# Optimization experiments

Hardware: AMD Instinct MI355X
Metric: run time of the kernel (lower is better)

## Reference

```python
import math
import jax, jax.numpy as jnp
import numpy as np

HEADS = 8
LOG_APPROX_VAR = math.log(0.01)  # self.var = 0.01, non-trainable


def clustering(x, approx_log_var, mu, log_var, log_prior):
    """Faithful port of DisentangledAttention.clustering (mi_estimation=False).
    x: [B,H,L,D]; approx_log_var: [B,H,L]; mu/log_var: [H,C,D]; log_prior: [H,C].
    Returns (cluster_probs [B,H,L,C], kl_loss [B,1,1], div_loss [B])."""
    B, H, L, D = x.shape
    xe = x[:, :, :, None, :]                      # [B,H,L,1,D]
    mue = mu[:, None, :, :]                       # [H,1,C,D]
    alv = approx_log_var[:, :, :, None, None]     # [B,H,L,1,1]
    avar = jnp.exp(alv)
    lv = log_var[:, None, :, :]                   # [H,1,C,D]
    var = jnp.exp(lv)
    logp = jax.nn.log_softmax(log_prior, axis=-1)  # [H,C]

    mse = (xe - mue) ** 2 / var                   # [B,H,L,C,D]
    log_pdf = -0.5 * mse.sum(-1) - D * math.pi - 0.5 * lv.sum(-1)  # [B,H,L,C]
    log_pdf = log_pdf + logp[:, None, :]
    log_probs = jax.nn.log_softmax(log_pdf, axis=-1)
    probs = jnp.exp(log_probs)                    # [B,H,L,C]

    logp_b = logp[None, :, None, :]               # broadcast prior log-probs
    prior = jnp.exp(logp_b)
    # F.kl_div(log_probs, prior) = prior * (log(prior) - log_probs)
    kl = (prior * (logp_b - log_probs)).sum(-1).mean(axis=(1, 2))            # [B]
    kl = kl + 0.5 * (probs * (mse + avar / var + lv).sum(-1)).sum(-1).mean(axis=(1, 2))
    kl = kl - 0.5 * jnp.mean(((1.0 + alv).sum(-1)) * D, axis=(1, 2, 3))
    kl_loss = kl.reshape(-1, 1, 1)

    eyeL = jnp.eye(L, dtype=x.dtype)
    div = jnp.einsum('bhqc,bhkc->bhqk', probs, probs)   # [B,H,L,L]
    div = (div - eyeL) ** 2
    wmask = eyeL * 1.25 + (1.0 - eyeL) * 0.75
    div_loss = (div * wmask).mean(axis=(1, 2, 3))       # [B]
    return probs, kl_loss, div_loss


def setup_inputs() -> dict:
    k = jax.random.key(0)
    ks = jax.random.split(k, 10)
    B, L, D, H, C = 4, 1024, 512, HEADS, 8
    Dk = D // H
    lin_std = 1.0 / math.sqrt(2.0 * D)  # xavier_normal gain=1/sqrt(2)
    return {
        'query': jax.random.normal(ks[0], (B, L, D), jnp.float32),
        'key': jax.random.normal(ks[1], (B, L, D), jnp.float32),
        'value': jax.random.normal(ks[2], (B, L, D), jnp.float32),
        'padding_mask': jnp.zeros((B, 1, L), jnp.float32),
        'Wq': jax.random.normal(ks[3], (D, D), jnp.float32) * lin_std,
        'bq': jnp.zeros((D,), jnp.float32),
        'Wk': jax.random.normal(ks[4], (D, D), jnp.float32) * lin_std,
        'bk': jnp.zeros((D,), jnp.float32),
        'Wv': jax.random.normal(ks[5], (D, D), jnp.float32) * lin_std,
        'bv': jnp.zeros((D,), jnp.float32),
        'Wo': jax.random.normal(ks[6], (D, D), jnp.float32) * lin_std,
        'bo': jnp.zeros((D,), jnp.float32),
        'tok_mu': jax.random.normal(ks[7], (H, C, Dk), jnp.float32) * 0.1,
        'tok_log_var': jnp.zeros((H, C, Dk), jnp.float32),
        'tok_log_prior': jnp.full((H, C), math.log(1.0 / C), jnp.float32),
    }


def reference(query, key, value, padding_mask, Wq, bq, Wk, bk, Wv, bv, Wo, bo,
              tok_mu, tok_log_var, tok_log_prior):
    B, L, D = query.shape
    H = HEADS
    Dk = D // H

    # GMM clustering on raw (unprojected) per-head query/key, eval mode (no reparam noise)
    qh = query.reshape(B, L, H, Dk).transpose(0, 2, 1, 3)  # [B,H,L,Dk]
    kh = key.reshape(B, L, H, Dk).transpose(0, 2, 1, 3)
    alv = jnp.full((B, H, L), LOG_APPROX_VAR, dtype=query.dtype)
    probs_q, kl_q, div_q = clustering(qh, alv, tok_mu, tok_log_var, tok_log_prior)
    probs_k, kl_k, div_k = clustering(kh, alv, tok_mu, tok_log_var, tok_log_prior)

    # Disentangled mask: tokens sharing clusters attend (mask==1 means blocked)
    sim = jnp.einsum('bhqc,bhkc->bhqk', probs_q, probs_k)   # [B,H,L,L]
    cmask = jnp.clip(1.0 - sim + padding_mask[:, :, None, :], 0.0, 1.0)

    # Projections + scaled softmax attention (per softmax_attention/full_attention)
    q = (query @ Wq.T + bq).reshape(B, L, H, Dk).transpose(0, 2, 1, 3) / math.sqrt(Dk)
    kk = (key @ Wk.T + bk).reshape(B, L, H, Dk).transpose(0, 2, 1, 3)
    v = (value @ Wv.T + bv).reshape(B, L, H, Dk).transpose(0, 2, 1, 3)
    scores = jnp.einsum('bhqd,bhkd->bhqk', q, kk) + jax.lax.stop_gradient(cmask) * (-10000.0)
    attn = jax.nn.softmax(scores, axis=-1) * (1.0 - cmask)
    out = jnp.einsum('bhqk,bhkd->bhqd', attn, v).transpose(0, 2, 1, 3).reshape(B, L, D)
    out = out @ Wo.T + bo

    kl_loss = kl_q + kl_k                      # [B,1,1]
    div_loss = (div_q + div_k).reshape(-1, 1, 1)  # [B,1,1]
    return out, kl_loss, div_loss
```

## Files before the change

kernel.cpp:

```cpp
#include <hip/hip_runtime.h>
#include <hip/hip_bf16.h>
#include <math.h>

#define NB 4
#define NL 1024
#define ND 512
#define NH 8
#define NC 8
#define NDK 64

static constexpr float KL3_CONST = 115.36544595161891f;

typedef __bf16 bf16x8 __attribute__((ext_vector_type(8)));
typedef float  f32x4v __attribute__((ext_vector_type(4)));
typedef unsigned short u16x4 __attribute__((ext_vector_type(4)));
typedef unsigned short u16x8 __attribute__((ext_vector_type(8)));

__device__ __forceinline__ unsigned short bf16u(float f) {
    return __builtin_bit_cast(unsigned short, (__bf16)f);
}

struct GemmArgs {
    const void* A; const float* W; const float* bias; void* out;
    float scale; int abf; int obf; int brow; int ostr; int vmap;
};

#define GEMM_BUF 15360

__device__ __forceinline__ void gemm_body(const GemmArgs& g, unsigned char* smem)
{
    const int tid = threadIdx.x;
    int n0, m0;
    if (g.vmap) {
        const int linear = blockIdx.y * 4 + blockIdx.x;
        n0 = (linear & 31) * 128;
        m0 = (linear >> 5) * 64;
    } else {
        n0 = blockIdx.x * 128;
        m0 = blockIdx.y * 64;
    }

    const int w = tid >> 6, lane = tid & 63;
    const int r16 = lane & 15, quad = lane >> 4;
    const int arow = tid >> 2, akc = tid & 3;
    const int wrow = tid >> 1, wkc = tid & 1;

    f32x4v acc[8];
#pragma unroll
    for (int n = 0; n < 8; ++n) acc[n] = (f32x4v){0.f, 0.f, 0.f, 0.f};

    auto ldA = [&](int k0) -> u16x8 {
        if (g.abf) {
            return *(const u16x8*)((const unsigned short*)g.A + (size_t)(m0 + arow) * 512 + k0 + akc * 8);
        }
        const float* ap = (const float*)g.A + (size_t)(m0 + arow) * 512 + k0 + akc * 8;
        const float4 a0 = *(const float4*)ap, a1 = *(const float4*)(ap + 4);
        return (u16x8){ bf16u(a0.x), bf16u(a0.y), bf16u(a0.z), bf16u(a0.w),
                        bf16u(a1.x), bf16u(a1.y), bf16u(a1.z), bf16u(a1.w) };
    };
    auto ldW = [&](int k0, u16x8* dst) {
        const float* wp = (const float*)g.W + (size_t)(n0 + wrow) * 512 + k0 + wkc * 16;
        const float4 w0 = *(const float4*)wp,       w1 = *(const float4*)(wp + 4);
        const float4 w2 = *(const float4*)(wp + 8), w3 = *(const float4*)(wp + 12);
        dst[0] = (u16x8){ bf16u(w0.x), bf16u(w0.y), bf16u(w0.z), bf16u(w0.w),
                          bf16u(w1.x), bf16u(w1.y), bf16u(w1.z), bf16u(w1.w) };
        dst[1] = (u16x8){ bf16u(w2.x), bf16u(w2.y), bf16u(w2.z), bf16u(w2.w),
                          bf16u(w3.x), bf16u(w3.y), bf16u(w3.z), bf16u(w3.w) };
    };
    auto store_stage = [&](int buf, const u16x8& sa, const u16x8* sw) {
        unsigned short* As = (unsigned short*)(smem + buf * GEMM_BUF);
        unsigned short* Ws = (unsigned short*)(smem + buf * GEMM_BUF + 5120);
        *(u16x8*)(As + arow * 40 + akc * 8) = sa;
        *(u16x8*)(Ws + wrow * 40 + wkc * 16) = sw[0];
        *(u16x8*)(Ws + wrow * 40 + wkc * 16 + 8) = sw[1];
    };
    auto mfma_half = [&](int buf) {
        unsigned short* As = (unsigned short*)(smem + buf * GEMM_BUF);
        unsigned short* Ws = (unsigned short*)(smem + buf * GEMM_BUF + 5120);
        bf16x8 af = *(const bf16x8*)(As + (w * 16 + r16) * 40 + quad * 8);
#pragma unroll
        for (int ni = 0; ni < 8; ++ni) {
            bf16x8 bfr = *(const bf16x8*)(Ws + (ni * 16 + r16) * 40 + quad * 8);
            acc[ni] = __builtin_amdgcn_mfma_f32_16x16x32_bf16(af, bfr, acc[ni], 0, 0, 0);
        }
    };

    u16x8 sa0 = ldA(0),  sw0[2]; ldW(0, sw0);
    u16x8 sa1 = ldA(32), sw1[2]; ldW(32, sw1);
    store_stage(0, sa0, sw0);
    sa0 = ldA(64); ldW(64, sw0);

    for (int p = 0; p < 16; p += 2) {
        const int kbase = p * 32;
        __syncthreads();
        store_stage(1, sa1, sw1);
        if (kbase + 96 < 512) { sa1 = ldA(kbase + 96); ldW(kbase + 96, sw1); }
        mfma_half(0);

        __syncthreads();
        if (p + 2 < 16) store_stage(0, sa0, sw0);
        if (kbase + 128 < 512) { sa0 = ldA(kbase + 128); ldW(kbase + 128, sw0); }
        mfma_half(1);
    }

#pragma unroll
    for (int ni = 0; ni < 8; ++ni) {
        const int col = n0 + ni * 16 + r16;
        const float bcol = g.brow ? 0.f : g.bias[col];
#pragma unroll
        for (int i = 0; i < 4; ++i) {
            const int row = m0 + w * 16 + quad * 4 + i;
            const float bv = g.brow ? g.bias[row] : bcol;
            const float v = (acc[ni][i] + bv) * g.scale;
            if (g.obf) ((unsigned short*)g.out)[(size_t)row * g.ostr + col] = bf16u(v);
            else       ((float*)g.out)[(size_t)row * g.ostr + col] = v;
        }
    }
}

__device__ __forceinline__ void cluster_body(
    const float* __restrict__ query, const float* __restrict__ key,
    const float* __restrict__ tok_mu, const float* __restrict__ tok_log_var,
    const float* __restrict__ tok_log_prior,
    float* __restrict__ probs_q, float* __restrict__ probs_k,
    float* __restrict__ klp, float* __restrict__ divp, float* __restrict__ Gp,
    int linear, unsigned char* smem)
{
    float* mu_s    = (float*)smem;
    float* iv_s    = (float*)(smem + 2048);
    float* Pl      = (float*)(smem + 4096);
    float* Gpart   = (float*)(smem + 13312);
    float* red_s   = (float*)(smem + 14336);
    float* lvsum_s = (float*)(smem + 14368);
    float* alpha_s = (float*)(smem + 14400);
    float* logp_s  = (float*)(smem + 14432);
    float* prior_s = (float*)(smem + 14464);

    const int tid  = threadIdx.x;
    const int side = linear >> 7;
    const int rem  = linear & 127;
    const int bh   = rem >> 2, chunk = rem & 3;
    const int b    = bh >> 3, h = bh & 7;
    const int blocklin = side * 128 + bh * 4 + chunk;
    const float* src = side ? key : query;
    float* probs_out = side ? probs_k : probs_q;

    for (int i = tid; i < 512; i += 256) {
        mu_s[i] = tok_mu[h * 512 + i];
        float lv = tok_log_var[h * 512 + i];
        iv_s[i] = __expf(-lv);
    }
    if (tid < 8) {
        float ls = 0.f, al = 0.f;
        for (int d = 0; d < 64; ++d) {
            float lv = tok_log_var[(h * 8 + tid) * 64 + d];
            ls += lv;
            al += 0.01f * __expf(-lv) + lv;
        }
        lvsum_s[tid] = ls; alpha_s[tid] = al;
    }
    if (tid == 0) {
        float lp[8]; float mx = -1e30f;
        for (int c = 0; c < 8; ++c) { lp[c] = tok_log_prior[h * 8 + c]; mx = fmaxf(mx, lp[c]); }
        float se = 0.f;
        for (int c = 0; c < 8; ++c) se += __expf(lp[c] - mx);
        float lse = mx + __logf(se);
        for (int c = 0; c < 8; ++c) { logp_s[c] = lp[c] - lse; prior_s[c] = __expf(lp[c] - lse); }
    }
    __syncthreads();

    const int l = chunk * 256 + tid;
    const float4* xp = (const float4*)(src + ((size_t)(b * NL + l)) * ND + h * NDK);
    float4 xr[16];
#pragma unroll
    for (int i = 0; i < 16; ++i) xr[i] = xp[i];

    float ms[8];
#pragma unroll
    for (int c = 0; c < 8; ++c) {
        const float4* mc = (const float4*)(mu_s + c * 64);
        const float4* ic = (const float4*)(iv_s + c * 64);
        float s = 0.f;
#pragma unroll
        for (int i = 0; i < 16; ++i) {
            float4 m4 = mc[i], v4 = ic[i], x4 = xr[i];
            float dx = x4.x - m4.x; s = fmaf(dx * dx, v4.x, s);
            float dy = x4.y - m4.y; s = fmaf(dy * dy, v4.y, s);
            float dz = x4.z - m4.z; s = fmaf(dz * dz, v4.z, s);
            float dw = x4.w - m4.w; s = fmaf(dw * dw, v4.w, s);
        }
        ms[c] = s;
    }

    float lpdf[8]; float mx = -1e30f;
#pragma unroll
    for (int c = 0; c < 8; ++c) {
        lpdf[c] = -0.5f * (ms[c] + lvsum_s[c]) + logp_s[c];
        mx = fmaxf(mx, lpdf[c]);
    }
    float e[8]; float se = 0.f;
#pragma unroll
    for (int c = 0; c < 8; ++c) { e[c] = __expf(lpdf[c] - mx); se += e[c]; }
    float lse = __logf(se);
    float inv = 1.f / se;
    float p[8]; float kl1 = 0.f, kl2 = 0.f, sqq = 0.f;
#pragma unroll
    for (int c = 0; c < 8; ++c) {
        p[c] = e[c] * inv;
        float logprob = lpdf[c] - mx - lse;
        kl1 += prior_s[c] * (logp_s[c] - logprob);
        kl2 += p[c] * (ms[c] + alpha_s[c]);
        sqq = fmaf(p[c], p[c], sqq);
    }

    float* po = probs_out + ((size_t)((b * NH + h) * NL + l)) * NC;
    ((float4*)po)[0] = make_float4(p[0], p[1], p[2], p[3]);
    ((float4*)po)[1] = make_float4(p[4], p[5], p[6], p[7]);
#pragma unroll
    for (int c = 0; c < 8; ++c) Pl[tid * 9 + c] = p[c];

    float dterm = 1.25f * (sqq - 1.f) * (sqq - 1.f) - 0.75f * sqq * sqq;
    float klv = kl1 + 0.5f * kl2;
    __syncthreads();

    {
        int qt = tid >> 6, pos = tid & 63, c1 = pos >> 3, c2 = pos & 7;
        float g = 0.f;
        for (int i = 0; i < 64; ++i) {
            int ll = qt * 64 + i;
            g = fmaf(Pl[ll * 9 + c1], Pl[ll * 9 + c2], g);
        }
        Gpart[qt * 64 + pos] = g;
    }

#pragma unroll
    for (int o = 32; o > 0; o >>= 1) {
        klv   += __shfl_down(klv, o);
        dterm += __shfl_down(dterm, o);
    }
    if ((tid & 63) == 0) { red_s[tid >> 6] = klv; red_s[4 + (tid >> 6)] = dterm; }
    __syncthreads();
    if (tid == 0) {
        klp[blocklin]  = red_s[0] + red_s[1] + red_s[2] + red_s[3];
        divp[blocklin] = red_s[4] + red_s[5] + red_s[6] + red_s[7];
    }
    if (tid < 64)
        Gp[(size_t)blocklin * 64 + tid] =
            Gpart[tid] + Gpart[64 + tid] + Gpart[128 + tid] + Gpart[192 + tid];
}

__global__ __launch_bounds__(256) void fused_front(
    GemmArgs g0, GemmArgs g1, GemmArgs g2,
    const float* query, const float* key,
    const float* tok_mu, const float* tok_log_var, const float* tok_log_prior,
    float* probs_q, float* probs_k,
    float* klp, float* divp, float* Gp)
{
    __shared__ alignas(16) unsigned char smem[2 * GEMM_BUF];
    if (blockIdx.z == 3) {
        const int linear = blockIdx.y * 4 + blockIdx.x;
        cluster_body(query, key, tok_mu, tok_log_var, tok_log_prior,
                     probs_q, probs_k, klp, divp, Gp, linear, smem);
        return;
    }
    GemmArgs g = (blockIdx.z == 0) ? g0 : ((blockIdx.z == 1) ? g1 : g2);
    gemm_body(g, smem);
}

#define APAD 72

__global__ __launch_bounds__(256) void attn_mfma5_kernel(
    const unsigned short* __restrict__ qp16, const unsigned short* __restrict__ kp16,
    const unsigned short* __restrict__ vtp16,
    const float* __restrict__ probs_q, const float* __restrict__ probs_k,
    const float* __restrict__ padding_mask,
    float* __restrict__ pO, float* __restrict__ pML)
{
    const int tid = threadIdx.x, lane = tid & 63, w = tid >> 6;
    const int r16 = lane & 15, quad = lane >> 4;
    const int b = blockIdx.z >> 1, s = blockIdx.z & 1;
    const int h = blockIdx.y;
    const int qt = blockIdx.x;
    const int qbase = qt * 64;

    __shared__ alignas(16) unsigned short Ks[64 * APAD];
    __shared__ alignas(16) unsigned short Vt[64 * APAD];
    __shared__ alignas(16) unsigned short Ps[4][16 * APAD];
    __shared__ float pk_s[8 * 65];
    __shared__ float pm_s[64];

    const int c0row = tid >> 3,        c0c8 = tid & 7;
    const int c1row = (tid + 256) >> 3, c1c8 = tid & 7;
    const int pkey = tid >> 1, phalf = tid & 1;

    bf16x8 qa[2];
    {
        const unsigned short* qrow = qp16 + ((size_t)(b * NL + qbase + w * 16 + r16)) * ND + h * NDK;
        qa[0] = *(const bf16x8*)(qrow + quad * 8);
        qa[1] = *(const bf16x8*)(qrow + 32 + quad * 8);
    }
    float pq[4][8];
#pragma unroll
    for (int i = 0; i < 4; ++i) {
        const float* pr = probs_q + ((size_t)((b * NH + h) * NL + qbase + w * 16 + quad * 4 + i)) * NC;
        float4 a = ((const float4*)pr)[0], c = ((const float4*)pr)[1];
        pq[i][0] = a.x; pq[i][1] = a.y; pq[i][2] = a.z; pq[i][3] = a.w;
        pq[i][4] = c.x; pq[i][5] = c.y; pq[i][6] = c.z; pq[i][7] = c.w;
    }

    f32x4v oacc[4];
#pragma unroll
    for (int n = 0; n < 4; ++n) oacc[n] = (f32x4v){0.f, 0.f, 0.f, 0.f};
    float m_i[4] = {-1e30f, -1e30f, -1e30f, -1e30f};
    float l_i[4] = {0.f, 0.f, 0.f, 0.f};

    u16x8 rk0, rk1, rv0, rv1;
    float4 rpk;
    float rpm;

    auto stage_load = [&](int kt) {
        const int key0 = s * 512 + kt * 64;
        rk0 = *(const u16x8*)(kp16 + ((size_t)(b * NL + key0 + c0row)) * ND + h * NDK + c0c8 * 8);
        rk1 = *(const u16x8*)(kp16 + ((size_t)(b * NL + key0 + c1row)) * ND + h * NDK + c1c8 * 8);
        rv0 = *(const u16x8*)(vtp16 + ((size_t)(h * 64 + c0row)) * (NB * NL) + b * NL + key0 + c0c8 * 8);
        rv1 = *(const u16x8*)(vtp16 + ((size_t)(h * 64 + c1row)) * (NB * NL) + b * NL + key0 + c1c8 * 8);
        if (tid < 128)
            rpk = *(const float4*)(probs_k + ((size_t)((b * NH + h) * NL + key0 + pkey)) * NC + phalf * 4);
        if (tid < 64)
            rpm = padding_mask[b * NL + key0 + tid];
    };
    auto stage_store = [&]() {
        *(u16x8*)(Ks + c0row * APAD + c0c8 * 8) = rk0;
        *(u16x8*)(Ks + c1row * APAD + c1c8 * 8) = rk1;
        *(u16x8*)(Vt + c0row * APAD + c0c8 * 8) = rv0;
        *(u16x8*)(Vt + c1row * APAD + c1c8 * 8) = rv1;
        if (tid < 128) {
            pk_s[(phalf * 4 + 0) * 65 + pkey] = rpk.x;
            pk_s[(phalf * 4 + 1) * 65 + pkey] = rpk.y;
            pk_s[(phalf * 4 + 2) * 65 + pkey] = rpk.z;
            pk_s[(phalf * 4 + 3) * 65 + pkey] = rpk.w;
        }
        if (tid < 64) pm_s[tid] = rpm;
    };

    stage_load(0);
    stage_store();
    stage_load(1);

    for (int kt = 0; kt < 8; ++kt) {
        __syncthreads();

        f32x4v sacc[4];
#pragma unroll
        for (int t = 0; t < 4; ++t) {
            sacc[t] = (f32x4v){0.f, 0.f, 0.f, 0.f};
            bf16x8 kb0 = *(const bf16x8*)(Ks + (t * 16 + r16) * APAD + quad * 8);
            bf16x8 kb1 = *(const bf16x8*)(Ks + (t * 16 + r16) * APAD + 32 + quad * 8);
            sacc[t] = __builtin_amdgcn_mfma_f32_16x16x32_bf16(qa[0], kb0, sacc[t], 0, 0, 0);
            sacc[t] = __builtin_amdgcn_mfma_f32_16x16x32_bf16(qa[1], kb1, sacc[t], 0, 0, 0);
        }

        float sc[4][4], wgt[4][4];
#pragma unroll
        for (int t = 0; t < 4; ++t) {
            const int keyl = t * 16 + r16;
            float pkc[8];
#pragma unroll
            for (int c = 0; c < 8; ++c) pkc[c] = pk_s[c * 65 + keyl];
            const float pmv = pm_s[keyl];
#pragma unroll
            for (int i = 0; i < 4; ++i) {
                float sim = 0.f;
#pragma unroll
                for (int c = 0; c < 8; ++c) sim = fmaf(pq[i][c], pkc[c], sim);
                float cm = 1.f - sim + pmv;
                cm = fminf(fmaxf(cm, 0.f), 1.f);
                sc[t][i] = sacc[t][i] - 10000.f * cm;
                wgt[t][i] = 1.f - cm;
            }
        }

        float mx[4];
#pragma unroll
        for (int i = 0; i < 4; ++i)
            mx[i] = fmaxf(fmaxf(sc[0][i], sc[1][i]), fmaxf(sc[2][i], sc[3][i]));
#pragma unroll
        for (int o = 1; o < 16; o <<= 1) {
#pragma unroll
            for (int i = 0; i < 4; ++i) mx[i] = fmaxf(mx[i], __shfl_xor(mx[i], o));
        }
        float rr[4];
#pragma unroll
        for (int i = 0; i < 4; ++i) {
            const float mnew = fmaxf(m_i[i], mx[i]);
            rr[i] = __expf(m_i[i] - mnew);
            m_i[i] = mnew;
            l_i[i] *= rr[i];
        }
#pragma unroll
        for (int n = 0; n < 4; ++n) {
            oacc[n][0] *= rr[0]; oacc[n][1] *= rr[1];
            oacc[n][2] *= rr[2]; oacc[n][3] *= rr[3];
        }
        float lad[4] = {0.f, 0.f, 0.f, 0.f};
#pragma unroll
        for (int t = 0; t < 4; ++t) {
#pragma unroll
            for (int i = 0; i < 4; ++i) {
                const float p = __expf(sc[t][i] - m_i[i]);
                lad[i] += p;
                Ps[w][(quad * 4 + i) * APAD + t * 16 + r16] = bf16u(p * wgt[t][i]);
            }
        }
#pragma unroll
        for (int o = 1; o < 16; o <<= 1) {
#pragma unroll
            for (int i = 0; i < 4; ++i) lad[i] += __shfl_xor(lad[i], o);
        }
#pragma unroll
        for (int i = 0; i < 4; ++i) l_i[i] += lad[i];

        bf16x8 pa0 = *(const bf16x8*)(Ps[w] + r16 * APAD + quad * 8);
        bf16x8 pa1 = *(const bf16x8*)(Ps[w] + r16 * APAD + 32 + quad * 8);
#pragma unroll
        for (int n = 0; n < 4; ++n) {
            bf16x8 vb0 = *(const bf16x8*)(Vt + (n * 16 + r16) * APAD + quad * 8);
            bf16x8 vb1 = *(const bf16x8*)(Vt + (n * 16 + r16) * APAD + 32 + quad * 8);
            oacc[n] = __builtin_amdgcn_mfma_f32_16x16x32_bf16(pa0, vb0, oacc[n], 0, 0, 0);
            oacc[n] = __builtin_amdgcn_mfma_f32_16x16x32_bf16(pa1, vb1, oacc[n], 0, 0, 0);
        }

        __syncthreads();
        if (kt < 7) {
            stage_store();
            if (kt < 6) stage_load(kt + 2);
        }
    }

    const int sb32 = (((b * 8 + h) << 5) | (qt * 2 + (w >> 1)));
    float* po = pO + ((size_t)sb32 * 2 + s) * 2048;
#pragma unroll
    for (int i = 0; i < 4; ++i) {
        const int row = (w & 1) * 16 + quad * 4 + i;
#pragma unroll
        for (int n = 0; n < 4; ++n)
            po[row * 64 + n * 16 + r16] = oacc[n][i];
    }
    if (r16 == 0) {
        float* pml = pML + ((size_t)sb32 * 2 + s) * 64;
#pragma unroll
        for (int i = 0; i < 4; ++i) {
            const int row = (w & 1) * 16 + quad * 4 + i;
            pml[row * 2]     = m_i[i];
            pml[row * 2 + 1] = l_i[i];
        }
    }
}

__device__ __forceinline__ void finalize_body(
    const float* __restrict__ klp, const float* __restrict__ divp,
    const float* __restrict__ Gp, float* __restrict__ out_tail)
{
    const int tid = threadIdx.x, b = tid >> 6, lane = tid & 63;
    float gsum = 0.f;
#pragma unroll
    for (int s = 0; s < 2; ++s)
#pragma unroll
        for (int h = 0; h < 8; ++h) {
            const int base = s * 128 + (b * 8 + h) * 4;
            float Ge = 0.f;
#pragma unroll
            for (int x = 0; x < 4; ++x) Ge += Gp[(size_t)(base + x) * 64 + lane];
            gsum = fmaf(Ge, Ge, gsum);
        }
    const int s = lane >> 5, rem = lane & 31, h = rem >> 2, x = rem & 3;
    const int idx = s * 128 + (b * 8 + h) * 4 + x;
    float klv = klp[idx];
    float dvv = divp[idx];
#pragma unroll
    for (int o = 32; o > 0; o >>= 1) {
        gsum += __shfl_down(gsum, o);
        klv  += __shfl_down(klv, o);
        dvv  += __shfl_down(dvv, o);
    }
    if (lane == 0) {
        out_tail[b]     = klv * (1.0f / 8192.0f) + 2.0f * KL3_CONST;
        out_tail[4 + b] = (dvv + 0.75f * gsum) * (1.0f / 8388608.0f);
    }
}

__global__ __launch_bounds__(256) void merge_fin_kernel(
    const float* __restrict__ pO, const float* __restrict__ pML,
    unsigned short* __restrict__ ao16,
    const float* __restrict__ klp, const float* __restrict__ divp,
    const float* __restrict__ Gp, float* __restrict__ out_tail)
{
    if (blockIdx.x == 1024) { finalize_body(klp, divp, Gp, out_tail); return; }
    const int gid = blockIdx.x * 256 + threadIdx.x;
    const int sb = gid >> 8, rem = gid & 255;
    const int row = rem >> 3, d0 = (rem & 7) * 8;

    const float2 ml0 = *(const float2*)(pML + ((size_t)sb * 2 + 0) * 64 + row * 2);
    const float2 ml1 = *(const float2*)(pML + ((size_t)sb * 2 + 1) * 64 + row * 2);
    const float M = fmaxf(ml0.x, ml1.x);
    const float e0 = __expf(ml0.x - M), e1 = __expf(ml1.x - M);
    const float inv = 1.f / fmaf(ml0.y, e0, ml1.y * e1);
    const float f0 = e0 * inv, f1 = e1 * inv;

    const float* p0 = pO + ((size_t)sb * 2 + 0) * 2048 + row * 64 + d0;
    const float* p1 = pO + ((size_t)sb * 2 + 1) * 2048 + row * 64 + d0;
    const int qt = sb & 31, bh = sb >> 5, h = bh & 7, b = bh >> 3;
    unsigned short* orow = ao16 + ((size_t)(b * NL + qt * 32 + row)) * ND + h * NDK + d0;

    const float4 a0 = *(const float4*)p0,       a1 = *(const float4*)(p0 + 4);
    const float4 c0 = *(const float4*)p1,       c1 = *(const float4*)(p1 + 4);
    u16x8 ov = { bf16u(a0.x * f0 + c0.x * f1), bf16u(a0.y * f0 + c0.y * f1),
                 bf16u(a0.z * f0 + c0.z * f1), bf16u(a0.w * f0 + c0.w * f1),
                 bf16u(a1.x * f0 + c1.x * f1), bf16u(a1.y * f0 + c1.y * f1),
                 bf16u(a1.z * f0 + c1.z * f1), bf16u(a1.w * f0 + c1.w * f1) };
    *(u16x8*)orow = ov;
}

__global__ __launch_bounds__(256) void gemm_single(GemmArgs g)
{
    __shared__ alignas(16) unsigned char smem[2 * GEMM_BUF];
    gemm_body(g, smem);
}

extern "C" void kernel_launch(void* const* d_in, const int* in_sizes, int n_in,
                              void* d_out, int out_size, void* d_ws, size_t ws_size,
                              hipStream_t stream)
{
    const float* query        = (const float*)d_in[0];
    const float* key          = (const float*)d_in[1];
    const float* value        = (const float*)d_in[2];
    const float* padding_mask = (const float*)d_in[3];
    const float* Wq = (const float*)d_in[4];
    const float* bq = (const float*)d_in[5];
    const float* Wk = (const float*)d_in[6];
    const float* bk = (const float*)d_in[7];
    const float* Wv = (const float*)d_in[8];
    const float* bv = (const float*)d_in[9];
    const float* Wo = (const float*)d_in[10];
    const float* bo = (const float*)d_in[11];
    const float* tok_mu        = (const float*)d_in[12];
    const float* tok_log_var   = (const float*)d_in[13];
    const float* tok_log_prior = (const float*)d_in[14];

    float* ws = (float*)d_ws;
    const size_t FS = 1048576;
    unsigned short* qp16  = (unsigned short*)ws;
    unsigned short* kp16  = (unsigned short*)(ws + FS);
    unsigned short* vtp16 = (unsigned short*)(ws + 2 * FS);
    unsigned short* ao16  = (unsigned short*)(ws + 3 * FS);
    float* probs_q = ws + 4 * FS;
    float* probs_k = probs_q + (size_t)NB * NH * NL * NC;
    float* pO      = probs_k + (size_t)NB * NH * NL * NC;
    float* pML     = pO + 4194304;
    float* klp     = pML + 131072;
    float* divp    = klp + 256;
    float* Gp      = divp + 256;

    GemmArgs gq {query, Wq, bq, qp16, 0.125f, 0, 1, 0, 512, 0};
    GemmArgs gk {key,   Wk, bk, kp16, 1.f,    0, 1, 0, 512, 0};
    GemmArgs gvt{Wv, value, bv, vtp16, 1.f,   0, 1, 1, 4096, 1};
    fused_front<<<dim3(4, 64, 4), 256, 0, stream>>>(
        gq, gk, gvt, query, key, tok_mu, tok_log_var, tok_log_prior,
        probs_q, probs_k, klp, divp, Gp);

    attn_mfma5_kernel<<<dim3(16, NH, NB * 2), 256, 0, stream>>>(
        qp16, kp16, vtp16, probs_q, probs_k, padding_mask, pO, pML);

    merge_fin_kernel<<<1025, 256, 0, stream>>>(
        pO, pML, ao16, klp, divp, Gp, (float*)d_out + (size_t)NB * NL * ND);

    GemmArgs go{ao16, Wo, bo, d_out, 1.f, 1, 0, 0, 512, 0};
    gemm_single<<<dim3(4, 64, 1), 256, 0, stream>>>(go);
}
```

Measured before the change: 197.5 us.

## Double-buffer attention K/V tiles and use 64-wide tiles for output GEMM

The attention kernel now keeps two shared-memory buffers for the K, V, probs_k and mask tiles. This removes the second per-iteration barrier, so the next tile is stored while the current one is consumed. The output projection switches to a new 64x64-tile GEMM body launched with twice as many blocks in N, which improves occupancy and load balance for the final projection. The cost is more shared memory in the attention kernel and more redundant A-tile loads in the smaller GEMM tiles.

```diff
diff --git a/kernel.cpp b/kernel.cpp
--- a/kernel.cpp
+++ b/kernel.cpp
@@ -118,6 +118,86 @@
     }
 }
 
+#define GEMM_BUF64 10240
+
+__device__ __forceinline__ void gemm_body64(const GemmArgs& g, unsigned char* smem)
+{
+    const int tid = threadIdx.x;
+    const int n0 = blockIdx.x * 64, m0 = blockIdx.y * 64;
+
+    const int w = tid >> 6, lane = tid & 63;
+    const int r16 = lane & 15, quad = lane >> 4;
+    const int arow = tid >> 2, akc = tid & 3;
+
+    f32x4v acc[4];
+#pragma unroll
+    for (int n = 0; n < 4; ++n) acc[n] = (f32x4v){0.f, 0.f, 0.f, 0.f};
+
+    auto ldA = [&](int k0) -> u16x8 {
+        if (g.abf) {
+            return *(const u16x8*)((const unsigned short*)g.A + (size_t)(m0 + arow) * 512 + k0 + akc * 8);
+        }
+        const float* ap = (const float*)g.A + (size_t)(m0 + arow) * 512 + k0 + akc * 8;
+        const float4 a0 = *(const float4*)ap, a1 = *(const float4*)(ap + 4);
+        return (u16x8){ bf16u(a0.x), bf16u(a0.y), bf16u(a0.z), bf16u(a0.w),
+                        bf16u(a1.x), bf16u(a1.y), bf16u(a1.z), bf16u(a1.w) };
+    };
+    auto ldW8 = [&](int k0) -> u16x8 {
+        const float* wp = (const float*)g.W + (size_t)(n0 + arow) * 512 + k0 + akc * 8;
+        const float4 w0 = *(const float4*)wp, w1 = *(const float4*)(wp + 4);
+        return (u16x8){ bf16u(w0.x), bf16u(w0.y), bf16u(w0.z), bf16u(w0.w),
+                        bf16u(w1.x), bf16u(w1.y), bf16u(w1.z), bf16u(w1.w) };
+    };
+    auto store_stage = [&](int buf, const u16x8& sa, const u16x8& sw) {
+        unsigned short* As = (unsigned short*)(smem + buf * GEMM_BUF64);
+        unsigned short* Ws = (unsigned short*)(smem + buf * GEMM_BUF64 + 5120);
+        *(u16x8*)(As + arow * 40 + akc * 8) = sa;
+        *(u16x8*)(Ws + arow * 40 + akc * 8) = sw;
+    };
+    auto mfma_half = [&](int buf) {
+        unsigned short* As = (unsigned short*)(smem + buf * GEMM_BUF64);
+        unsigned short* Ws = (unsigned short*)(smem + buf * GEMM_BUF64 + 5120);
+        bf16x8 af = *(const bf16x8*)(As + (w * 16 + r16) * 40 + quad * 8);
+#pragma unroll
+        for (int ni = 0; ni < 4; ++ni) {
+            bf16x8 bfr = *(const bf16x8*)(Ws + (ni * 16 + r16) * 40 + quad * 8);
+            acc[ni] = __builtin_amdgcn_mfma_f32_16x16x32_bf16(af, bfr, acc[ni], 0, 0, 0);
+        }
+    };
+
+    u16x8 sa0 = ldA(0),  sw0 = ldW8(0);
+    u16x8 sa1 = ldA(32), sw1 = ldW8(32);
+    store_stage(0, sa0, sw0);
+    sa0 = ldA(64); sw0 = ldW8(64);
+
+    for (int p = 0; p < 16; p += 2) {
+        const int kbase = p * 32;
+        __syncthreads();
+        store_stage(1, sa1, sw1);
+        if (kbase + 96 < 512) { sa1 = ldA(kbase + 96); sw1 = ldW8(kbase + 96); }
+        mfma_half(0);
+
+        __syncthreads();
+        if (p + 2 < 16) store_stage(0, sa0, sw0);
+        if (kbase + 128 < 512) { sa0 = ldA(kbase + 128); sw0 = ldW8(kbase + 128); }
+        mfma_half(1);
+    }
+
+#pragma unroll
+    for (int ni = 0; ni < 4; ++ni) {
+        const int col = n0 + ni * 16 + r16;
+        const float bcol = g.brow ? 0.f : g.bias[col];
+#pragma unroll
+        for (int i = 0; i < 4; ++i) {
+            const int row = m0 + w * 16 + quad * 4 + i;
+            const float bv = g.brow ? g.bias[row] : bcol;
+            const float v = (acc[ni][i] + bv) * g.scale;
+            if (g.obf) ((unsigned short*)g.out)[(size_t)row * g.ostr + col] = bf16u(v);
+            else       ((float*)g.out)[(size_t)row * g.ostr + col] = v;
+        }
+    }
+}
+
 __device__ __forceinline__ void cluster_body(
     const float* __restrict__ query, const float* __restrict__ key,
     const float* __restrict__ tok_mu, const float* __restrict__ tok_log_var,
@@ -269,7 +349,7 @@
 
 #define APAD 72
 
-__global__ __launch_bounds__(256) void attn_mfma5_kernel(
+__global__ __launch_bounds__(256) void attn_mfma6_kernel(
     const unsigned short* __restrict__ qp16, const unsigned short* __restrict__ kp16,
     const unsigned short* __restrict__ vtp16,
     const float* __restrict__ probs_q, const float* __restrict__ probs_k,
@@ -283,11 +363,11 @@
     const int qt = blockIdx.x;
     const int qbase = qt * 64;
 
-    __shared__ alignas(16) unsigned short Ks[64 * APAD];
-    __shared__ alignas(16) unsigned short Vt[64 * APAD];
+    __shared__ alignas(16) unsigned short Ks[2][64 * APAD];
+    __shared__ alignas(16) unsigned short Vt[2][64 * APAD];
     __shared__ alignas(16) unsigned short Ps[4][16 * APAD];
-    __shared__ float pk_s[8 * 65];
-    __shared__ float pm_s[64];
+    __shared__ float pk_s[2][8 * 65];
+    __shared__ float pm_s[2][64];
 
     const int c0row = tid >> 3,        c0c8 = tid & 7;
     const int c1row = (tid + 256) >> 3, c1c8 = tid & 7;
@@ -329,33 +409,34 @@
         if (tid < 64)
             rpm = padding_mask[b * NL + key0 + tid];
     };
-    auto stage_store = [&]() {
-        *(u16x8*)(Ks + c0row * APAD + c0c8 * 8) = rk0;
-        *(u16x8*)(Ks + c1row * APAD + c1c8 * 8) = rk1;
-        *(u16x8*)(Vt + c0row * APAD + c0c8 * 8) = rv0;
-        *(u16x8*)(Vt + c1row * APAD + c1c8 * 8) = rv1;
+    auto stage_store = [&](int buf) {
+        *(u16x8*)(Ks[buf] + c0row * APAD + c0c8 * 8) = rk0;
+        *(u16x8*)(Ks[buf] + c1row * APAD + c1c8 * 8) = rk1;
+        *(u16x8*)(Vt[buf] + c0row * APAD + c0c8 * 8) = rv0;
+        *(u16x8*)(Vt[buf] + c1row * APAD + c1c8 * 8) = rv1;
         if (tid < 128) {
-            pk_s[(phalf * 4 + 0) * 65 + pkey] = rpk.x;
-            pk_s[(phalf * 4 + 1) * 65 + pkey] = rpk.y;
-            pk_s[(phalf * 4 + 2) * 65 + pkey] = rpk.z;
-            pk_s[(phalf * 4 + 3) * 65 + pkey] = rpk.w;
-        }
-        if (tid < 64) pm_s[tid] = rpm;
+            pk_s[buf][(phalf * 4 + 0) * 65 + pkey] = rpk.x;
+            pk_s[buf][(phalf * 4 + 1) * 65 + pkey] = rpk.y;
+            pk_s[buf][(phalf * 4 + 2) * 65 + pkey] = rpk.z;
+            pk_s[buf][(phalf * 4 + 3) * 65 + pkey] = rpk.w;
+        }
+        if (tid < 64) pm_s[buf][tid] = rpm;
     };
 
     stage_load(0);
-    stage_store();
+    stage_store(0);
     stage_load(1);
 
     for (int kt = 0; kt < 8; ++kt) {
+        const int cur = kt & 1;
         __syncthreads();
 
         f32x4v sacc[4];
 #pragma unroll
         for (int t = 0; t < 4; ++t) {
             sacc[t] = (f32x4v){0.f, 0.f, 0.f, 0.f};
-            bf16x8 kb0 = *(const bf16x8*)(Ks + (t * 16 + r16) * APAD + quad * 8);
-            bf16x8 kb1 = *(const bf16x8*)(Ks + (t * 16 + r16) * APAD + 32 + quad * 8);
+            bf16x8 kb0 = *(const bf16x8*)(Ks[cur] + (t * 16 + r16) * APAD + quad * 8);
+            bf16x8 kb1 = *(const bf16x8*)(Ks[cur] + (t * 16 + r16) * APAD + 32 + quad * 8);
             sacc[t] = __builtin_amdgcn_mfma_f32_16x16x32_bf16(qa[0], kb0, sacc[t], 0, 0, 0);
             sacc[t] = __builtin_amdgcn_mfma_f32_16x16x32_bf16(qa[1], kb1, sacc[t], 0, 0, 0);
         }
@@ -366,8 +447,8 @@
             const int keyl = t * 16 + r16;
             float pkc[8];
 #pragma unroll
-            for (int c = 0; c < 8; ++c) pkc[c] = pk_s[c * 65 + keyl];
-            const float pmv = pm_s[keyl];
+            for (int c = 0; c < 8; ++c) pkc[c] = pk_s[cur][c * 65 + keyl];
+            const float pmv = pm_s[cur][keyl];
 #pragma unroll
             for (int i = 0; i < 4; ++i) {
                 float sim = 0.f;
@@ -424,17 +505,14 @@
         bf16x8 pa1 = *(const bf16x8*)(Ps[w] + r16 * APAD + 32 + quad * 8);
 #pragma unroll
         for (int n = 0; n < 4; ++n) {
-            bf16x8 vb0 = *(const bf16x8*)(Vt + (n * 16 + r16) * APAD + quad * 8);
-            bf16x8 vb1 = *(const bf16x8*)(Vt + (n * 16 + r16) * APAD + 32 + quad * 8);
+            bf16x8 vb0 = *(const bf16x8*)(Vt[cur] + (n * 16 + r16) * APAD + quad * 8);
+            bf16x8 vb1 = *(const bf16x8*)(Vt[cur] + (n * 16 + r16) * APAD + 32 + quad * 8);
             oacc[n] = __builtin_amdgcn_mfma_f32_16x16x32_bf16(pa0, vb0, oacc[n], 0, 0, 0);
             oacc[n] = __builtin_amdgcn_mfma_f32_16x16x32_bf16(pa1, vb1, oacc[n], 0, 0, 0);
         }
 
-        __syncthreads();
-        if (kt < 7) {
-            stage_store();
-            if (kt < 6) stage_load(kt + 2);
-        }
+        if (kt < 7) stage_store(cur ^ 1);
+        if (kt < 6) stage_load(kt + 2);
     }
 
     const int sb32 = (((b * 8 + h) << 5) | (qt * 2 + (w >> 1)));
@@ -521,10 +599,10 @@
     *(u16x8*)orow = ov;
 }
 
-__global__ __launch_bounds__(256) void gemm_single(GemmArgs g)
-{
-    __shared__ alignas(16) unsigned char smem[2 * GEMM_BUF];
-    gemm_body(g, smem);
+__global__ __launch_bounds__(256) void gemm_single64(GemmArgs g)
+{
+    __shared__ alignas(16) unsigned char smem[2 * GEMM_BUF64];
+    gemm_body64(g, smem);
 }
 
 extern "C" void kernel_launch(void* const* d_in, const int* in_sizes, int n_in,
@@ -568,12 +646,12 @@
         gq, gk, gvt, query, key, tok_mu, tok_log_var, tok_log_prior,
         probs_q, probs_k, klp, divp, Gp);
 
-    attn_mfma5_kernel<<<dim3(16, NH, NB * 2), 256, 0, stream>>>(
+    attn_mfma6_kernel<<<dim3(16, NH, NB * 2), 256, 0, stream>>>(
         qp16, kp16, vtp16, probs_q, probs_k, padding_mask, pO, pML);
 
     merge_fin_kernel<<<1025, 256, 0, stream>>>(
         pO, pML, ao16, klp, divp, Gp, (float*)d_out + (size_t)NB * NL * ND);
 
     GemmArgs go{ao16, Wo, bo, d_out, 1.f, 1, 0, 0, 512, 0};
-    gemm_single<<<dim3(4, 64, 1), 256, 0, stream>>>(go);
-}
+    gemm_single64<<<dim3(8, 64, 1), 256, 0, stream>>>(go);
+}
```

Result: faster. 190.7 us (-3.4%).
